# Kernel optimization log

Measured on AMD Instinct MI355X. Metric: run time of the kernel, lower is better.

## Reference

```python
import jax, jax.numpy as jnp
import numpy as np

GRID = 4
N = GRID * GRID  # 16 nodes
CIN = 16
HID = 64
HEADS = 4
OUT = 256
NEG_SLOPE = 0.2  # PyG GATConv default leaky relu slope
LN_EPS = 1e-5


def _adj_mask():
    # 4-connected grid adjacency + self loops (PyG GATConv add_self_loops=True)
    m = np.zeros((N, N), dtype=bool)
    for i in range(GRID):
        for j in range(GRID):
            u = i * GRID + j
            if j + 1 < GRID:
                v = i * GRID + j + 1
                m[u, v] = m[v, u] = True
            if i + 1 < GRID:
                v = (i + 1) * GRID + j
                m[u, v] = m[v, u] = True
    np.fill_diagonal(m, True)
    return m

ADJ = jnp.asarray(_adj_mask())  # [N, N], adj[i, j] = j is a (self-)neighbor of i


def gat_layer(h, W, a_src, a_dst, b, concat):
    """PyG GATConv on the fixed grid graph, dense-masked form.
    h: [B, N, Fin]; W: [Fin, HEADS*C]; a_src/a_dst: [HEADS, C]."""
    B = h.shape[0]
    H, C = a_src.shape
    wh = (h @ W).reshape(B, N, H, C)                       # [B, N, H, C]
    e_src = jnp.einsum('bnhc,hc->bnh', wh, a_src)          # alpha_src . Wh_j
    e_dst = jnp.einsum('bnhc,hc->bnh', wh, a_dst)          # alpha_dst . Wh_i
    # score[b, i, j, h]: target i attends to source j
    e = e_dst[:, :, None, :] + e_src[:, None, :, :]
    e = jax.nn.leaky_relu(e, NEG_SLOPE)
    e = jnp.where(ADJ[None, :, :, None], e, -1e9)
    alpha = jax.nn.softmax(e, axis=2)                      # softmax over sources j
    out = jnp.einsum('bijh,bjhc->bihc', alpha, wh)         # [B, N, H, C]
    if concat:
        out = out.reshape(B, N, H * C)
    else:
        out = out.mean(axis=2)
    return out + b


def setup_inputs() -> dict:
    key = jax.random.key(0)
    ks = jax.random.split(key, 24)
    s = 0.05
    B = 16384
    inp = {
        'x': jax.random.normal(ks[0], (B, CIN, GRID, GRID), dtype=jnp.float32),
        'w_in': jax.random.normal(ks[1], (CIN, HID), dtype=jnp.float32) * s,
        'b_in': jnp.zeros((HID,), jnp.float32),
        # GAT layer 0: in 64 -> 4 heads x 64, concat
        'W0': jax.random.normal(ks[2], (HID, HEADS * HID), dtype=jnp.float32) * s,
        'asrc0': jax.random.normal(ks[3], (HEADS, HID), dtype=jnp.float32) * s,
        'adst0': jax.random.normal(ks[4], (HEADS, HID), dtype=jnp.float32) * s,
        'bb0': jnp.zeros((HEADS * HID,), jnp.float32),
        # GAT layer 1: in 256 -> 4 heads x 64, concat
        'W1': jax.random.normal(ks[5], (HEADS * HID, HEADS * HID), dtype=jnp.float32) * s,
        'asrc1': jax.random.normal(ks[6], (HEADS, HID), dtype=jnp.float32) * s,
        'adst1': jax.random.normal(ks[7], (HEADS, HID), dtype=jnp.float32) * s,
        'bb1': jnp.zeros((HEADS * HID,), jnp.float32),
        # GAT layer 2: in 256 -> 4 heads x 64, mean over heads (concat=False)
        'W2': jax.random.normal(ks[8], (HEADS * HID, HEADS * HID), dtype=jnp.float32) * s,
        'asrc2': jax.random.normal(ks[9], (HEADS, HID), dtype=jnp.float32) * s,
        'adst2': jax.random.normal(ks[10], (HEADS, HID), dtype=jnp.float32) * s,
        'bb2': jnp.zeros((HID,), jnp.float32),
        # output MLP: 64 -> 128 (LN, ReLU) -> 256
        'w1': jax.random.normal(ks[11], (HID, OUT // 2), dtype=jnp.float32) * s,
        'b1': jnp.zeros((OUT // 2,), jnp.float32),
        'ln_g': jnp.ones((OUT // 2,), jnp.float32),
        'ln_b': jnp.zeros((OUT // 2,), jnp.float32),
        'w2': jax.random.normal(ks[12], (OUT // 2, OUT), dtype=jnp.float32) * s,
        'b2': jnp.zeros((OUT,), jnp.float32),
    }
    return inp


def reference(x, w_in, b_in, W0, asrc0, adst0, bb0, W1, asrc1, adst1, bb1,
              W2, asrc2, adst2, bb2, w1, b1, ln_g, ln_b, w2, b2):
    B = x.shape[0]
    # grid_to_graph: (B, C, H, W) -> (B, N, C) node features
    h = jnp.transpose(x, (0, 2, 3, 1)).reshape(B, N, CIN)
    h = jax.nn.relu(h @ w_in + b_in)
    h = gat_layer(h, W0, asrc0, adst0, bb0, concat=True)
    h = jax.nn.relu(h)  # dropout is identity at inference
    h = gat_layer(h, W1, asrc1, adst1, bb1, concat=True)
    h = jax.nn.relu(h)
    h = gat_layer(h, W2, asrc2, adst2, bb2, concat=False)  # [B, N, 64]
    g = h.mean(axis=1)  # global_mean_pool over the 16 nodes of each graph
    # MLP with LayerNorm
    y = g @ w1 + b1
    mu = y.mean(axis=-1, keepdims=True)
    var = ((y - mu) ** 2).mean(axis=-1, keepdims=True)
    y = (y - mu) * jax.lax.rsqrt(var + LN_EPS) * ln_g + ln_b
    y = jax.nn.relu(y)
    return y @ w2 + b2
```

## Files before the change

kernel.cpp:

```cpp
#include <hip/hip_runtime.h>
#include <hip/hip_bf16.h>

typedef short s8v __attribute__((ext_vector_type(8)));
typedef short s4v __attribute__((ext_vector_type(4)));
typedef float f4v __attribute__((ext_vector_type(4)));

#define WSTR 36
#define AP   20
#define HIXBASE(s, quad) (((s)*4 + (quad))*256)

__device__ constexpr unsigned KMASK[16] = {
  0x0013u,0x0027u,0x004Eu,0x008Cu,
  0x0131u,0x0272u,0x04E4u,0x08C8u,
  0x1310u,0x2720u,0x4E40u,0x8C80u,
  0x3100u,0x7200u,0xE400u,0xC800u};

__device__ __forceinline__ short f2b(float x){
  __hip_bfloat16 h = __float2bfloat16(x);
  return *reinterpret_cast<short*>(&h);
}
__device__ __forceinline__ float b2f(short s){
  __hip_bfloat16 h = *reinterpret_cast<__hip_bfloat16*>(&s);
  return __bfloat162float(h);
}
__device__ __forceinline__ unsigned pk2(float a, float b){
  unsigned ua = __float_as_uint(a), ub = __float_as_uint(b);
  ua += 0x7fffu + ((ua >> 16) & 1u);
  ub += 0x7fffu + ((ub >> 16) & 1u);
  return __builtin_amdgcn_perm(ub, ua, 0x07060302);
}

__global__ __launch_bounds__(256) void prep_all(
  const float* __restrict__ W0, const float* __restrict__ as0, const float* __restrict__ ad0,
  const float* __restrict__ W1, const float* __restrict__ as1, const float* __restrict__ ad1,
  const float* __restrict__ W2, const float* __restrict__ as2, const float* __restrict__ ad2,
  const float* __restrict__ w_in,
  short* __restrict__ ws)
{
  short* WPin = ws;
  short* WP0  = ws + 2048;
  short* WP1  = ws + 2048 + 17408;
  short* WP2  = ws + 2048 + 17408 + 69632;

  const int t = threadIdx.x, l = t & 63;
  const int gid = blockIdx.x*4 + (t >> 6);

  if (gid < 288){
    const float* W; short* WP; int u = gid, f, s, KS;
    if (u < 32)      { W = W0; WP = WP0; KS = 2; f = u >> 1; s = u & 1; }
    else if (u < 160){ u -= 32;  W = W1; WP = WP1; KS = 8; f = u >> 3; s = u & 7; }
    else             { u -= 160; W = W2; WP = WP2; KS = 8; f = u >> 3; s = u & 7; }
    const int lq = l & 15, quad = l >> 4;
    union { s8v v; short s16[8]; } o;
    #pragma unroll
    for (int j = 0; j < 8; ++j)
      o.s16[j] = f2b(W[(s*32 + quad*8 + j)*256 + f*16 + lq]);
    *(s8v*)(WP + ((f*KS + s)*64 + l)*8) = o.v;
  } else if (gid < 292){
    const int f = gid - 288;
    const int lq = l & 15, quad = l >> 4;
    union { s8v v; short s16[8]; } o;
    #pragma unroll
    for (int j = 0; j < 8; ++j){
      const int k = quad*8 + j;
      o.s16[j] = (k < 16) ? f2b(w_in[k*64 + f*16 + lq]) : (short)0;
    }
    *(s8v*)(WPin + (f*64 + l)*8) = o.v;
  } else {
    int u = gid - 292;
    const float* W; const float* as; const float* ad; short* WP; int KS, k;
    if (u < 64)      { W=W0; as=as0; ad=ad0; WP=WP0; KS=2; k=u; }
    else if (u < 320){ u-=64;  W=W1; as=as1; ad=ad1; WP=WP1; KS=8; k=u; }
    else             { u-=320; W=W2; as=as2; ad=ad2; WP=WP2; KS=8; k=u; }
    float v[8];
    #pragma unroll
    for (int h = 0; h < 4; ++h){
      const float wv_ = W[k*256 + h*64 + l];
      v[h]   = wv_ * as[h*64 + l];
      v[4+h] = wv_ * ad[h*64 + l];
    }
    #pragma unroll
    for (int s = 1; s < 64; s <<= 1)
      #pragma unroll
      for (int uu = 0; uu < 8; ++uu) v[uu] += __shfl_xor(v[uu], s, 64);
    if (l < 16){
      const float r = (l < 8) ? v[l] : 0.f;
      WP[((16*KS + (k >> 5))*64 + ((k >> 3) & 3)*16 + l)*8 + (k & 7)] = f2b(r);
    }
  }
}

template<int KS, bool MEAN>
__device__ __forceinline__ void gat_layer(short* bufH, short* whT, short* alphaS,
    const short* __restrict__ WP, const float* __restrict__ bbias,
    float* __restrict__ out, const int b, const int t)
{
  const int l = t & 63, wv = t >> 6, lq = l & 15, quad = l >> 4;
  {
    f4v acc[5][2];
    #pragma unroll
    for (int fi = 0; fi < 5; ++fi)
      #pragma unroll
      for (int nt = 0; nt < 2; ++nt) acc[fi][nt] = (f4v){0.f,0.f,0.f,0.f};
    #pragma unroll
    for (int s = 0; s < KS; ++s){
      const s8v a0 = *(const s8v*)&bufH[HIXBASE(s, quad) + lq*8];
      const s8v a1 = *(const s8v*)&bufH[HIXBASE(s, quad) + (16 + lq)*8];
      #pragma unroll
      for (int fi = 0; fi < 5; ++fi){
        if (fi == 4 && wv != 3) break;
        const int f = (fi == 4) ? 16 : fi*4 + wv;
        const s8v bF = *(const s8v*)&WP[((f*KS + s)*64 + l)*8];
        acc[fi][0] = __builtin_amdgcn_mfma_f32_16x16x32_bf16(a0, bF, acc[fi][0], 0,0,0);
        acc[fi][1] = __builtin_amdgcn_mfma_f32_16x16x32_bf16(a1, bF, acc[fi][1], 0,0,0);
      }
    }
    #pragma unroll
    for (int fi = 0; fi < 5; ++fi){
      if (fi == 4 && (wv != 3 || lq >= 8)) break;
      const int f = (fi == 4) ? 16 : fi*4 + wv;
      #pragma unroll
      for (int nt = 0; nt < 2; ++nt){
        uint2 p;
        p.x = pk2(acc[fi][nt][0], acc[fi][nt][1]);
        p.y = pk2(acc[fi][nt][2], acc[fi][nt][3]);
        *(uint2*)&whT[(f*16 + lq)*WSTR + nt*16 + quad*4] = p;
      }
    }
  }
  __syncthreads();
  if (t < 128){
    const int g = t >> 6, h = (t >> 4) & 3, i = t & 15;
    const float ed = b2f(whT[(260 + h)*WSTR + g*16 + i]);
    float ev[16];
    #pragma unroll
    for (int c = 0; c < 4; ++c){
      const s4v v = *(const s4v*)&whT[(256 + h)*WSTR + g*16 + c*4];
      ev[c*4+0]=b2f(v[0]); ev[c*4+1]=b2f(v[1]); ev[c*4+2]=b2f(v[2]); ev[c*4+3]=b2f(v[3]);
    }
    const unsigned m = KMASK[i];
    float ssum = 0.f;
    #pragma unroll
    for (int j = 0; j < 16; ++j){
      float e = ed + ev[j];
      e = (e > 0.f) ? e : 0.2f*e;
      const float a = ((m >> j) & 1u) ? __expf(e) : 0.f;
      ev[j] = a; ssum += a;
    }
    const float inv = 1.f / ssum;
    unsigned* row = (unsigned*)&alphaS[((g*4 + h)*16 + i)*AP];
    #pragma unroll
    for (int c = 0; c < 8; ++c)
      row[c] = pk2(ev[2*c]*inv, ev[2*c+1]*inv);
  }
  __syncthreads();
  if constexpr (!MEAN){
    const int h = wv;
    union { s8v v; unsigned u[4]; } B[2];
    #pragma unroll
    for (int g = 0; g < 2; ++g){
      const unsigned* ar = (const unsigned*)&alphaS[((g*4 + h)*16 + lq)*AP + (quad & 1)*8];
      const bool act = ((quad >> 1) == g);
      #pragma unroll
      for (int c = 0; c < 4; ++c) B[g].u[c] = act ? ar[c] : 0u;
    }
    #pragma unroll
    for (int ct = 0; ct < 4; ++ct){
      const s8v a = *(const s8v*)&whT[(h*64 + ct*16 + lq)*WSTR + quad*8];
      const int sf = h*2 + (ct >> 1);
      const int qf = (ct & 1)*2 + (quad >> 1);
      const int jf = (quad & 1)*4;
      const int f0 = h*64 + ct*16 + quad*4;
      const float4 bb = *(const float4*)&bbias[f0];
      #pragma unroll
      for (int g = 0; g < 2; ++g){
        f4v d = (f4v){0.f,0.f,0.f,0.f};
        d = __builtin_amdgcn_mfma_f32_16x16x32_bf16(a, B[g].v, d, 0,0,0);
        uint2 p;
        p.x = pk2(fmaxf(d[0] + bb.x, 0.f), fmaxf(d[1] + bb.y, 0.f));
        p.y = pk2(fmaxf(d[2] + bb.z, 0.f), fmaxf(d[3] + bb.w, 0.f));
        *(uint2*)&bufH[HIXBASE(sf, qf) + (g*16 + lq)*8 + jf] = p;
      }
    }
  } else {
    const int g = wv >> 1;
    union { s8v v; unsigned u[4]; } B[4];
    #pragma unroll
    for (int h = 0; h < 4; ++h){
      const unsigned* ar = (const unsigned*)&alphaS[((g*4 + h)*16 + lq)*AP + (quad & 1)*8];
      const bool act = ((quad >> 1) == g);
      #pragma unroll
      for (int c = 0; c < 4; ++c) B[h].u[c] = act ? ar[c] : 0u;
    }
    #pragma unroll
    for (int cc = 0; cc < 2; ++cc){
      const int ct = (wv & 1)*2 + cc;
      f4v d = (f4v){0.f,0.f,0.f,0.f};
      #pragma unroll
      for (int h = 0; h < 4; ++h){
        const s8v a = *(const s8v*)&whT[(h*64 + ct*16 + lq)*WSTR + quad*8];
        d = __builtin_amdgcn_mfma_f32_16x16x32_bf16(a, B[h].v, d, 0,0,0);
      }
      #pragma unroll
      for (int s = 1; s < 16; s <<= 1){
        d[0] += __shfl_xor(d[0], s, 64); d[1] += __shfl_xor(d[1], s, 64);
        d[2] += __shfl_xor(d[2], s, 64); d[3] += __shfl_xor(d[3], s, 64);
      }
      if (lq == 0){
        const int f0 = ct*16 + quad*4;
        const float4 bb = *(const float4*)&bbias[f0];
        float4 gv;
        gv.x = d[0]*(1.f/64.f) + bb.x; gv.y = d[1]*(1.f/64.f) + bb.y;
        gv.z = d[2]*(1.f/64.f) + bb.z; gv.w = d[3]*(1.f/64.f) + bb.w;
        *(float4*)&out[((size_t)b*2 + g)*256 + f0] = gv;
      }
    }
  }
}

__global__ __launch_bounds__(256, 4) void gat_main(
  const float* __restrict__ x,
  const short* __restrict__ WPin, const float* __restrict__ b_in,
  const short* __restrict__ WP0,  const float* __restrict__ bb0,
  const short* __restrict__ WP1,  const float* __restrict__ bb1,
  const short* __restrict__ WP2,  const float* __restrict__ bb2,
  float* __restrict__ out)
{
  __shared__ __align__(16) short smem[8*4*32*8 + 264*WSTR + 8*16*AP];
  short* bufH   = smem;
  short* whT    = smem + 8192;
  short* alphaS = smem + 8192 + 264*WSTR;
  short* h0     = whT;
  constexpr int H0S = 40;

  const int b = blockIdx.x;
  const int t = threadIdx.x;
  const int l = t & 63, wv = t >> 6, lq = l & 15, quad = l >> 4;

  {
    const float2 v = *(const float2*)&x[b*512 + 2*t];
    const int i0 = 2*t;
    const int g = i0 >> 8, c = (i0 >> 4) & 15, n = i0 & 15;
    h0[(g*16 + n)*H0S + c]     = f2b(v.x);
    h0[(g*16 + n + 1)*H0S + c] = f2b(v.y);
    const int r = t >> 3, cc = 16 + 2*(t & 7);
    h0[r*H0S + cc] = 0; h0[r*H0S + cc + 1] = 0;
  }
  __syncthreads();

  {
    const s8v aF  = *(const s8v*)&WPin[(wv*64 + l)*8];
    const s8v b0v = *(const s8v*)&h0[lq*H0S + quad*8];
    const s8v b1v = *(const s8v*)&h0[(16+lq)*H0S + quad*8];
    f4v acc0 = (f4v){0.f,0.f,0.f,0.f}, acc1 = (f4v){0.f,0.f,0.f,0.f};
    acc0 = __builtin_amdgcn_mfma_f32_16x16x32_bf16(aF, b0v, acc0, 0,0,0);
    acc1 = __builtin_amdgcn_mfma_f32_16x16x32_bf16(aF, b1v, acc1, 0,0,0);
    const int f0 = wv*16 + quad*4;
    const float4 bi = *(const float4*)&b_in[f0];
    const int sf = wv >> 1;
    const int qf = (wv & 1)*2 + (quad >> 1);
    const int jf = (quad & 1)*4;
    uint2 p0, p1;
    p0.x = pk2(fmaxf(acc0[0]+bi.x,0.f), fmaxf(acc0[1]+bi.y,0.f));
    p0.y = pk2(fmaxf(acc0[2]+bi.z,0.f), fmaxf(acc0[3]+bi.w,0.f));
    p1.x = pk2(fmaxf(acc1[0]+bi.x,0.f), fmaxf(acc1[1]+bi.y,0.f));
    p1.y = pk2(fmaxf(acc1[2]+bi.z,0.f), fmaxf(acc1[3]+bi.w,0.f));
    *(uint2*)&bufH[HIXBASE(sf, qf) + lq*8 + jf]        = p0;
    *(uint2*)&bufH[HIXBASE(sf, qf) + (16 + lq)*8 + jf] = p1;
  }
  __syncthreads();

  gat_layer<2, false>(bufH, whT, alphaS, WP0, bb0, out, b, t);
  __syncthreads();
  gat_layer<8, false>(bufH, whT, alphaS, WP1, bb1, out, b, t);
  __syncthreads();
  gat_layer<8, true >(bufH, whT, alphaS, WP2, bb2, out, b, t);
}

__global__ __launch_bounds__(256, 8) void mlp_tail(
  const float* __restrict__ w1,  const float* __restrict__ b1,
  const float* __restrict__ lng, const float* __restrict__ lnb,
  const float* __restrict__ w2,  const float* __restrict__ b2,
  float* __restrict__ out)
{
  __shared__ float ylds[256];
  __shared__ float red[8];
  const int b = blockIdx.x;
  const int t = threadIdx.x;
  const int gg = t >> 7, o = t & 127;
  const float* gptr = out + ((size_t)b*2 + gg)*256;

  float yv = b1[o];
  #pragma unroll 8
  for (int k = 0; k < 64; ++k) yv += gptr[k] * w1[k*128 + o];
  float s1 = yv, s2 = yv*yv;
  #pragma unroll
  for (int s = 1; s < 64; s <<= 1){ s1 += __shfl_xor(s1, s, 64); s2 += __shfl_xor(s2, s, 64); }
  if ((t & 63) == 0){ red[(t>>6)*2] = s1; red[(t>>6)*2 + 1] = s2; }
  __syncthreads();
  {
    const float S1 = red[4*gg] + red[4*gg+2], S2 = red[4*gg+1] + red[4*gg+3];
    const float mu  = S1 * (1.f/128.f);
    const float var = S2 * (1.f/128.f) - mu*mu;
    const float yn  = (yv - mu) * rsqrtf(var + 1e-5f) * lng[o] + lnb[o];
    ylds[gg*128 + o] = fmaxf(yn, 0.f);
  }
  __syncthreads();
  float a0 = b2[t], a1 = b2[t];
  #pragma unroll 4
  for (int k = 0; k < 128; ++k){
    const float wv2 = w2[k*256 + t];
    a0 += ylds[k]*wv2; a1 += ylds[128 + k]*wv2;
  }
  out[((size_t)b*2 + 0)*256 + t] = a0;
  out[((size_t)b*2 + 1)*256 + t] = a1;
}

extern "C" void kernel_launch(void* const* d_in, const int* in_sizes, int n_in,
                              void* d_out, int out_size, void* d_ws, size_t ws_size,
                              hipStream_t stream){
  const float* x    = (const float*)d_in[0];
  const float* w_in = (const float*)d_in[1];
  const float* b_in = (const float*)d_in[2];
  const float* W0   = (const float*)d_in[3];
  const float* as0  = (const float*)d_in[4];
  const float* ad0  = (const float*)d_in[5];
  const float* bb0  = (const float*)d_in[6];
  const float* W1   = (const float*)d_in[7];
  const float* as1  = (const float*)d_in[8];
  const float* ad1  = (const float*)d_in[9];
  const float* bb1  = (const float*)d_in[10];
  const float* W2   = (const float*)d_in[11];
  const float* as2  = (const float*)d_in[12];
  const float* ad2  = (const float*)d_in[13];
  const float* bb2  = (const float*)d_in[14];
  const float* w1   = (const float*)d_in[15];
  const float* b1   = (const float*)d_in[16];
  const float* lng  = (const float*)d_in[17];
  const float* lnb  = (const float*)d_in[18];
  const float* w2   = (const float*)d_in[19];
  const float* b2   = (const float*)d_in[20];
  const int B = in_sizes[0] / 256;

  short* ws = (short*)d_ws;
  const short* WPin = ws;
  const short* WP0  = ws + 2048;
  const short* WP1  = ws + 2048 + 17408;
  const short* WP2  = ws + 2048 + 17408 + 69632;

  prep_all<<<217, 256, 0, stream>>>(W0, as0, ad0, W1, as1, ad1, W2, as2, ad2,
                                    w_in, ws);
  gat_main<<<B/2, 256, 0, stream>>>(x, WPin, b_in, WP0, bb0, WP1, bb1, WP2, bb2,
                                    (float*)d_out);
  mlp_tail<<<B/2, 256, 0, stream>>>(w1, b1, lng, lnb, w2, b2, (float*)d_out);
}
```

Measured before the change: 336.6 us.

## Batch 32 graphs per MLP tail block to reuse weights from registers

```diff
diff --git a/kernel.cpp b/kernel.cpp
--- a/kernel.cpp
+++ b/kernel.cpp
@@ -277,43 +277,107 @@
   gat_layer<8, true >(bufH, whT, alphaS, WP2, bb2, out, b, t);
 }
 
-__global__ __launch_bounds__(256, 8) void mlp_tail(
+__global__ __launch_bounds__(256) void mlp_tail(
   const float* __restrict__ w1,  const float* __restrict__ b1,
   const float* __restrict__ lng, const float* __restrict__ lnb,
   const float* __restrict__ w2,  const float* __restrict__ b2,
   float* __restrict__ out)
 {
-  __shared__ float ylds[256];
-  __shared__ float red[8];
-  const int b = blockIdx.x;
+  __shared__ __align__(16) float gbuf[32*64];
+  __shared__ __align__(16) float yb[32*128];
+  __shared__ float red[64];
   const int t = threadIdx.x;
-  const int gg = t >> 7, o = t & 127;
-  const float* gptr = out + ((size_t)b*2 + gg)*256;
-
-  float yv = b1[o];
-  #pragma unroll 8
-  for (int k = 0; k < 64; ++k) yv += gptr[k] * w1[k*128 + o];
-  float s1 = yv, s2 = yv*yv;
+  const size_t gbase = (size_t)blockIdx.x * 32;
+
   #pragma unroll
-  for (int s = 1; s < 64; s <<= 1){ s1 += __shfl_xor(s1, s, 64); s2 += __shfl_xor(s2, s, 64); }
-  if ((t & 63) == 0){ red[(t>>6)*2] = s1; red[(t>>6)*2 + 1] = s2; }
-  __syncthreads();
-  {
-    const float S1 = red[4*gg] + red[4*gg+2], S2 = red[4*gg+1] + red[4*gg+3];
-    const float mu  = S1 * (1.f/128.f);
-    const float var = S2 * (1.f/128.f) - mu*mu;
-    const float yn  = (yv - mu) * rsqrtf(var + 1e-5f) * lng[o] + lnb[o];
-    ylds[gg*128 + o] = fmaxf(yn, 0.f);
-  }
-  __syncthreads();
-  float a0 = b2[t], a1 = b2[t];
-  #pragma unroll 4
-  for (int k = 0; k < 128; ++k){
-    const float wv2 = w2[k*256 + t];
-    a0 += ylds[k]*wv2; a1 += ylds[128 + k]*wv2;
-  }
-  out[((size_t)b*2 + 0)*256 + t] = a0;
-  out[((size_t)b*2 + 1)*256 + t] = a1;
+  for (int u = 0; u < 2; ++u){
+    const int id = u*256 + t;
+    const int gr = id >> 4, c4 = id & 15;
+    const float4 v = *(const float4*)&out[(gbase + gr)*256 + c4*4];
+    *(float4*)&gbuf[gr*64 + c4*4] = v;
+  }
+  __syncthreads();
+
+  const int o = t & 127, gs = t >> 7;
+  float w1c[64];
+  #pragma unroll
+  for (int k = 0; k < 64; ++k) w1c[k] = w1[k*128 + o];
+  const float b1v = b1[o];
+  float y[16];
+  #pragma unroll
+  for (int i = 0; i < 16; ++i){
+    const int gr = gs*16 + i;
+    float acc = b1v;
+    #pragma unroll
+    for (int k4 = 0; k4 < 16; ++k4){
+      const float4 gv = *(const float4*)&gbuf[gr*64 + k4*4];
+      acc += gv.x*w1c[k4*4] + gv.y*w1c[k4*4+1] + gv.z*w1c[k4*4+2] + gv.w*w1c[k4*4+3];
+    }
+    y[i] = acc;
+    yb[gr*128 + o] = acc;
+  }
+  __syncthreads();
+
+  {
+    const int gr = t >> 3, s = t & 7;
+    float s1 = 0.f, s2 = 0.f;
+    #pragma unroll
+    for (int c4 = 0; c4 < 4; ++c4){
+      const float4 v = *(const float4*)&yb[gr*128 + s*16 + c4*4];
+      s1 += v.x + v.y + v.z + v.w;
+      s2 += v.x*v.x + v.y*v.y + v.z*v.z + v.w*v.w;
+    }
+    #pragma unroll
+    for (int d = 1; d < 8; d <<= 1){
+      s1 += __shfl_xor(s1, d, 64);
+      s2 += __shfl_xor(s2, d, 64);
+    }
+    if (s == 0){
+      const float mu  = s1 * (1.f/128.f);
+      const float var = s2 * (1.f/128.f) - mu*mu;
+      red[gr*2]     = mu;
+      red[gr*2 + 1] = rsqrtf(var + 1e-5f);
+    }
+  }
+  __syncthreads();
+
+  {
+    const float lg = lng[o], lb = lnb[o];
+    #pragma unroll
+    for (int i = 0; i < 16; ++i){
+      const int gr = gs*16 + i;
+      const float yn = (y[i] - red[gr*2]) * red[gr*2 + 1] * lg + lb;
+      yb[gr*128 + o] = fmaxf(yn, 0.f);
+    }
+  }
+  __syncthreads();
+
+  {
+    const float b2v = b2[t];
+    #pragma unroll
+    for (int gh = 0; gh < 2; ++gh){
+      float acc[16];
+      #pragma unroll
+      for (int g = 0; g < 16; ++g) acc[g] = b2v;
+      #pragma unroll
+      for (int kh = 0; kh < 2; ++kh){
+        float w2c[64];
+        #pragma unroll
+        for (int k = 0; k < 64; ++k) w2c[k] = w2[(kh*64 + k)*256 + t];
+        #pragma unroll
+        for (int k4 = 0; k4 < 16; ++k4){
+          #pragma unroll
+          for (int g = 0; g < 16; ++g){
+            const float4 yv = *(const float4*)&yb[(gh*16 + g)*128 + kh*64 + k4*4];
+            acc[g] += yv.x*w2c[k4*4] + yv.y*w2c[k4*4+1] + yv.z*w2c[k4*4+2] + yv.w*w2c[k4*4+3];
+          }
+        }
+      }
+      #pragma unroll
+      for (int g = 0; g < 16; ++g)
+        out[(gbase + gh*16 + g)*256 + t] = acc[g];
+    }
+  }
 }
 
 extern "C" void kernel_launch(void* const* d_in, const int* in_sizes, int n_in,
@@ -352,5 +416,5 @@
                                     w_in, ws);
   gat_main<<<B/2, 256, 0, stream>>>(x, WPin, b_in, WP0, bb0, WP1, bb1, WP2, bb2,
                                     (float*)d_out);
-  mlp_tail<<<B/2, 256, 0, stream>>>(w1, b1, lng, lnb, w2, b2, (float*)d_out);
-}
+  mlp_tail<<<B/32, 256, 0, stream>>>(w1, b1, lng, lnb, w2, b2, (float*)d_out);
+}
```

Result: faster. 324.8 us (-3.5%).
